# Kernel tuning notes

Measured on AMD Instinct MI355X. Metric: run time of the kernel, lower is better.

The kernel has to match this reference:

```python
import jax, jax.numpy as jnp
import numpy as np

B, N, D = 4, 4096, 3
Q = jnp.array([0.05, 0.95, 0.25, 0.75], dtype=jnp.float32)  # q_begin + q_end


def _nn_diff(S1, S2):
    # For each point in S1 find nearest point in S2 (squared L2), return S1 - closest_S2.
    # d2: [N, N] built via the ||a||^2 + ||b||^2 - 2ab expansion (avoids [N,N,D]).
    d2 = (jnp.sum(S1 * S1, axis=-1, keepdims=True)
          + jnp.sum(S2 * S2, axis=-1)[None, :]
          - 2.0 * (S1 @ S2.T))
    idx = jnp.argmin(d2, axis=1)          # [N] nearest index in S2
    return S1 - S2[idx]                   # [N, D] vector residuals (mean=False path)


def _masked_std(v, mask):
    # torch.std over the masked subset (unbiased, correction=1), mask is float {0,1}.
    n = jnp.sum(mask)
    mean = jnp.sum(v * mask) / n
    var = jnp.sum(mask * (v - mean) ** 2) / (n - 1.0)
    return jnp.sqrt(var)


def _mask_std_pair(d):
    # mask_by_Z: quantiles computed under no_grad (stop_gradient), then std of each subset.
    v = d.reshape(-1)
    q = jnp.quantile(jax.lax.stop_gradient(v), Q.astype(v.dtype))
    mask_begin = ((v < q[0]) | (v > q[1])).astype(v.dtype)
    mask_end = ((v > q[2]) & (v < q[3])).astype(v.dtype)
    return _masked_std(v, mask_begin), _masked_std(v, mask_end)


def _sigma_distance(S1, S2):
    d12 = _nn_diff(S1, S2)  # S1 -> S2 residuals
    d21 = _nn_diff(S2, S1)  # S2 -> S1 residuals
    b1, e1 = _mask_std_pair(d12)
    b2, e2 = _mask_std_pair(d21)
    return jnp.maximum(b1, b2), jnp.maximum(e1, e2)


def setup_inputs() -> dict:
    key = jax.random.key(0)
    kx, ky = jax.random.split(key)
    x = jax.random.normal(kx, (B, N, D), dtype=jnp.float32)
    y = jax.random.normal(ky, (B, N, D), dtype=jnp.float32)
    return {"x": x, "y": y}


def reference(x, y):
    begin, end = jax.vmap(_sigma_distance)(x, y)  # [B], [B]
    return begin.mean(), end.mean()
```

## Files before the change

kernel.cpp:

```cpp
#include <hip/hip_runtime.h>
#include <math.h>

constexpr int B_  = 4;
constexpr int N_  = 4096;
constexpr int NV  = N_ * 3;
constexpr int CCHUNK = 1024;
constexpr int NCH = N_ / CCHUNK;

__device__ inline unsigned f2k(float f) {
    unsigned b = __float_as_uint(f);
    return b ^ ((unsigned)((int)b >> 31) | 0x80000000u);
}
__device__ inline float k2f(unsigned k) {
    unsigned b = (k & 0x80000000u) ? (k ^ 0x80000000u) : ~k;
    return __uint_as_float(b);
}

__global__ __launch_bounds__(256) void nn_partial_kernel(const float* __restrict__ x,
                                                         const float* __restrict__ y,
                                                         float2* __restrict__ part) {
    __shared__ float4 s2[CCHUNK];
    const int pair = blockIdx.z;
    const int b    = pair >> 1;
    const int dir  = pair & 1;
    const float* S1 = (dir == 0 ? x : y) + b * NV;
    const float* S2 = (dir == 0 ? y : x) + b * NV;
    const int cbase = blockIdx.y * CCHUNK;

    for (int j = threadIdx.x; j < CCHUNK; j += 256) {
        float bx = S2[(cbase + j) * 3 + 0];
        float by = S2[(cbase + j) * 3 + 1];
        float bz = S2[(cbase + j) * 3 + 2];
        s2[j] = make_float4(bx, by, bz, bx * bx + by * by + bz * bz);
    }
    __syncthreads();

    const int q = blockIdx.x * 256 + threadIdx.x;
    const float ax = S1[q * 3 + 0];
    const float ay = S1[q * 3 + 1];
    const float az = S1[q * 3 + 2];

    float best = INFINITY;
    int bidx = 0;
    #pragma unroll 8
    for (int j = 0; j < CCHUNK; ++j) {
        float4 c = s2[j];
        float dot = ax * c.x + ay * c.y + az * c.z;
        float d2  = fmaf(-2.0f, dot, c.w);
        if (d2 < best) { best = d2; bidx = cbase + j; }
    }
    part[(pair * NCH + blockIdx.y) * N_ + q] = make_float2(best, (float)bidx);
}

__global__ __launch_bounds__(256) void nn_merge_kernel(const float* __restrict__ x,
                                                       const float* __restrict__ y,
                                                       const float2* __restrict__ part,
                                                       float* __restrict__ resid) {
    const int pair = blockIdx.y;
    const int b    = pair >> 1;
    const int dir  = pair & 1;
    const float* S1 = (dir == 0 ? x : y) + b * NV;
    const float* S2 = (dir == 0 ? y : x) + b * NV;
    const int q = blockIdx.x * 256 + threadIdx.x;

    float best = INFINITY;
    int bidx = 0;
    #pragma unroll
    for (int c = 0; c < NCH; ++c) {
        float2 p = part[(pair * NCH + c) * N_ + q];
        if (p.x < best) { best = p.x; bidx = (int)p.y; }
    }
    float* outp = resid + pair * NV + q * 3;
    outp[0] = S1[q * 3 + 0] - S2[bidx * 3 + 0];
    outp[1] = S1[q * 3 + 1] - S2[bidx * 3 + 1];
    outp[2] = S1[q * 3 + 2] - S2[bidx * 3 + 2];
}

__global__ __launch_bounds__(1024) void quantile_select_kernel(const float* __restrict__ resid,
                                                               float* __restrict__ qbuf) {
    __shared__ unsigned keys[NV];
    __shared__ int hist[256];
    __shared__ int s_sel, s_want, s_cnt;
    __shared__ unsigned s_min;

    const int t    = blockIdx.x & 3;
    const int pair = blockIdx.x >> 2;
    const int tid  = threadIdx.x;
    const float* v = resid + pair * NV;

    const float Qs[4] = {0.05f, 0.95f, 0.25f, 0.75f};
    const float pos = Qs[t] * (float)(NV - 1);
    const int   k0  = (int)floorf(pos);
    const float fr  = pos - (float)k0;

    for (int i = tid; i < NV; i += 1024) keys[i] = f2k(v[i]);
    __syncthreads();

    unsigned prefix = 0u, pmask = 0u;
    int want = k0;
    for (int shift = 24; shift >= 0; shift -= 8) {
        for (int i = tid; i < 256; i += 1024) hist[i] = 0;
        __syncthreads();
        for (int i = tid; i < NV; i += 1024) {
            unsigned k = keys[i];
            if ((k & pmask) == prefix) atomicAdd(&hist[(k >> shift) & 255], 1);
        }
        __syncthreads();
        if (tid < 64) {
            int c0 = hist[tid * 4 + 0], c1 = hist[tid * 4 + 1];
            int c2 = hist[tid * 4 + 2], c3 = hist[tid * 4 + 3];
            int s = c0 + c1 + c2 + c3;
            int pre = s;
            #pragma unroll
            for (int off = 1; off < 64; off <<= 1) {
                int u = __shfl_up(pre, off);
                if (tid >= off) pre += u;
            }
            int excl = pre - s;
            bool hit = (want >= excl) && (want < excl + s);
            unsigned long long m = __ballot(hit);
            int hl = (int)(__ffsll((unsigned long long)m) - 1);
            if (tid == hl) {
                int w = want - excl;
                int sel;
                if      (w < c0)           { sel = tid * 4 + 0; }
                else if (w < c0 + c1)      { sel = tid * 4 + 1; w -= c0; }
                else if (w < c0 + c1 + c2) { sel = tid * 4 + 2; w -= c0 + c1; }
                else                       { sel = tid * 4 + 3; w -= c0 + c1 + c2; }
                s_sel = sel; s_want = w;
            }
        }
        __syncthreads();
        prefix |= ((unsigned)s_sel) << shift;
        pmask  |= (0xFFu << shift);
        want = s_want;
        __syncthreads();
    }
    const unsigned key0 = prefix;
    const float v0 = k2f(key0);

    if (tid == 0) { s_cnt = 0; s_min = 0xFFFFFFFFu; }
    __syncthreads();
    int loc = 0; unsigned locmin = 0xFFFFFFFFu;
    for (int i = tid; i < NV; i += 1024) {
        unsigned k = keys[i];
        if (k <= key0) loc++;
        else if (k < locmin) locmin = k;
    }
    atomicAdd(&s_cnt, loc);
    atomicMin(&s_min, locmin);
    __syncthreads();
    if (tid == 0) {
        float v1 = (s_cnt >= k0 + 2) ? v0 : k2f(s_min);
        qbuf[pair * 4 + t] = v0 + fr * (v1 - v0);
    }
}

__global__ __launch_bounds__(1024) void masked_stats_kernel(const float* __restrict__ resid,
                                                            const float* __restrict__ qbuf,
                                                            float* __restrict__ stats) {
    __shared__ float red[64];
    __shared__ float sh[8];
    const int pair = blockIdx.x;
    const int tid  = threadIdx.x;
    const float* v = resid + pair * NV;
    const float q0 = qbuf[pair * 4 + 0], q1 = qbuf[pair * 4 + 1];
    const float q2 = qbuf[pair * 4 + 2], q3 = qbuf[pair * 4 + 3];

    float cb = 0.f, sb = 0.f, ce = 0.f, se = 0.f;
    for (int i = tid; i < NV; i += 1024) {
        float val = v[i];
        if ((val < q0) || (val > q1)) { cb += 1.f; sb += val; }
        if ((val > q2) && (val < q3)) { ce += 1.f; se += val; }
    }
    for (int off = 32; off > 0; off >>= 1) {
        cb += __shfl_down(cb, off);
        sb += __shfl_down(sb, off);
        ce += __shfl_down(ce, off);
        se += __shfl_down(se, off);
    }
    const int wid = tid >> 6, lane = tid & 63;
    if (lane == 0) {
        red[wid * 4 + 0] = cb; red[wid * 4 + 1] = sb;
        red[wid * 4 + 2] = ce; red[wid * 4 + 3] = se;
    }
    __syncthreads();
    if (tid == 0) {
        float tcb = 0.f, tsb = 0.f, tce = 0.f, tse = 0.f;
        for (int w = 0; w < 16; ++w) {
            tcb += red[w * 4 + 0]; tsb += red[w * 4 + 1];
            tce += red[w * 4 + 2]; tse += red[w * 4 + 3];
        }
        sh[0] = tsb / tcb;
        sh[1] = tse / tce;
        sh[2] = tcb;
        sh[3] = tce;
    }
    __syncthreads();
    const float mean_b = sh[0], mean_e = sh[1];
    const float nb = sh[2], ne = sh[3];

    float vb = 0.f, ve = 0.f;
    for (int i = tid; i < NV; i += 1024) {
        float val = v[i];
        if ((val < q0) || (val > q1)) { float d = val - mean_b; vb += d * d; }
        if ((val > q2) && (val < q3)) { float d = val - mean_e; ve += d * d; }
    }
    for (int off = 32; off > 0; off >>= 1) {
        vb += __shfl_down(vb, off);
        ve += __shfl_down(ve, off);
    }
    __syncthreads();
    if (lane == 0) { red[wid * 2 + 0] = vb; red[wid * 2 + 1] = ve; }
    __syncthreads();
    if (tid == 0) {
        float tvb = 0.f, tve = 0.f;
        for (int w = 0; w < 16; ++w) { tvb += red[w * 2 + 0]; tve += red[w * 2 + 1]; }
        stats[pair * 2 + 0] = sqrtf(tvb / (nb - 1.f));
        stats[pair * 2 + 1] = sqrtf(tve / (ne - 1.f));
    }
}

__global__ void final_kernel(const float* __restrict__ stats, float* __restrict__ out) {
    if (threadIdx.x == 0 && blockIdx.x == 0) {
        float sb = 0.f, se = 0.f;
        for (int b = 0; b < B_; ++b) {
            float b1 = stats[(b * 2 + 0) * 2 + 0];
            float b2 = stats[(b * 2 + 1) * 2 + 0];
            float e1 = stats[(b * 2 + 0) * 2 + 1];
            float e2 = stats[(b * 2 + 1) * 2 + 1];
            sb += fmaxf(b1, b2);
            se += fmaxf(e1, e2);
        }
        out[0] = sb / (float)B_;
        out[1] = se / (float)B_;
    }
}

extern "C" void kernel_launch(void* const* d_in, const int* in_sizes, int n_in,
                              void* d_out, int out_size, void* d_ws, size_t ws_size,
                              hipStream_t stream) {
    const float* x = (const float*)d_in[0];
    const float* y = (const float*)d_in[1];
    float* out = (float*)d_out;

    float*  resid = (float*)d_ws;
    float2* part  = (float2*)(resid + 8 * NV);
    float*  qbuf  = (float*)(part + 8 * NCH * N_);
    float*  stats = qbuf + 32;

    nn_partial_kernel<<<dim3(N_ / 256, NCH, 8), 256, 0, stream>>>(x, y, part);
    nn_merge_kernel<<<dim3(N_ / 256, 8), 256, 0, stream>>>(x, y, part, resid);
    quantile_select_kernel<<<32, 1024, 0, stream>>>(resid, qbuf);
    masked_stats_kernel<<<8, 1024, 0, stream>>>(resid, qbuf, stats);
    final_kernel<<<1, 64, 0, stream>>>(stats, out);
}
```

Baseline: 73.41 us.

## Register-tile NN search with 8 queries per thread and adaptive candidate split

The nearest-neighbour kernel now has each thread hold 8 query points in registers, loaded with float4 reads, and reuse every shared-memory candidate across all 8. Candidates are pre-scaled by -2 so the distance is a chain of three FMAs. The candidate dimension is split into up to 32 chunks, picked at launch from the workspace size, so the grid keeps enough blocks. The quantile and stats kernels drop to 256 threads, use vectorized float4 loads and reduce with wave shuffles instead of per-thread shared atomics. The costs are higher register pressure and a longer partial-result merge when there are more chunks.

```diff
diff --git a/kernel.cpp b/kernel.cpp
--- a/kernel.cpp
+++ b/kernel.cpp
@@ -4,8 +4,7 @@
 constexpr int B_  = 4;
 constexpr int N_  = 4096;
 constexpr int NV  = N_ * 3;
-constexpr int CCHUNK = 1024;
-constexpr int NCH = N_ / CCHUNK;
+constexpr int QPT = 8;
 
 __device__ inline unsigned f2k(float f) {
     unsigned b = __float_as_uint(f);
@@ -18,44 +17,69 @@
 
 __global__ __launch_bounds__(256) void nn_partial_kernel(const float* __restrict__ x,
                                                          const float* __restrict__ y,
-                                                         float2* __restrict__ part) {
-    __shared__ float4 s2[CCHUNK];
+                                                         float2* __restrict__ part,
+                                                         int ncch) {
+    __shared__ float4 s2[1024];
+    const int cch  = N_ / ncch;
     const int pair = blockIdx.z;
     const int b    = pair >> 1;
     const int dir  = pair & 1;
     const float* S1 = (dir == 0 ? x : y) + b * NV;
     const float* S2 = (dir == 0 ? y : x) + b * NV;
-    const int cbase = blockIdx.y * CCHUNK;
-
-    for (int j = threadIdx.x; j < CCHUNK; j += 256) {
+    const int cbase = blockIdx.x * cch;
+
+    for (int j = threadIdx.x; j < cch; j += 256) {
         float bx = S2[(cbase + j) * 3 + 0];
         float by = S2[(cbase + j) * 3 + 1];
         float bz = S2[(cbase + j) * 3 + 2];
-        s2[j] = make_float4(bx, by, bz, bx * bx + by * by + bz * bz);
-    }
-    __syncthreads();
-
-    const int q = blockIdx.x * 256 + threadIdx.x;
-    const float ax = S1[q * 3 + 0];
-    const float ay = S1[q * 3 + 1];
-    const float az = S1[q * 3 + 2];
-
-    float best = INFINITY;
-    int bidx = 0;
-    #pragma unroll 8
-    for (int j = 0; j < CCHUNK; ++j) {
+        s2[j] = make_float4(-2.f * bx, -2.f * by, -2.f * bz,
+                            bx * bx + by * by + bz * bz);
+    }
+    __syncthreads();
+
+    const int q0 = blockIdx.y * 2048 + threadIdx.x * QPT;
+    float ax[QPT], ay[QPT], az[QPT];
+    {
+        const float4* p4 = (const float4*)(S1 + q0 * 3);
+        float4 v[6];
+        #pragma unroll
+        for (int i = 0; i < 6; ++i) v[i] = p4[i];
+        const float* f = (const float*)v;
+        #pragma unroll
+        for (int k = 0; k < QPT; ++k) {
+            ax[k] = f[k * 3 + 0]; ay[k] = f[k * 3 + 1]; az[k] = f[k * 3 + 2];
+        }
+    }
+
+    float best[QPT]; int idx[QPT];
+    #pragma unroll
+    for (int k = 0; k < QPT; ++k) { best[k] = INFINITY; idx[k] = 0; }
+
+    #pragma unroll 2
+    for (int j = 0; j < cch; ++j) {
         float4 c = s2[j];
-        float dot = ax * c.x + ay * c.y + az * c.z;
-        float d2  = fmaf(-2.0f, dot, c.w);
-        if (d2 < best) { best = d2; bidx = cbase + j; }
-    }
-    part[(pair * NCH + blockIdx.y) * N_ + q] = make_float2(best, (float)bidx);
+        const int jg = cbase + j;
+        #pragma unroll
+        for (int k = 0; k < QPT; ++k) {
+            float d2 = fmaf(ax[k], c.x, fmaf(ay[k], c.y, fmaf(az[k], c.z, c.w)));
+            if (d2 < best[k]) idx[k] = jg;
+            best[k] = fminf(d2, best[k]);
+        }
+    }
+
+    float2 o[QPT];
+    #pragma unroll
+    for (int k = 0; k < QPT; ++k) o[k] = make_float2(best[k], (float)idx[k]);
+    float4* op = (float4*)(part + (size_t)(pair * ncch + blockIdx.x) * N_ + q0);
+    #pragma unroll
+    for (int i = 0; i < QPT / 2; ++i) op[i] = ((const float4*)o)[i];
 }
 
 __global__ __launch_bounds__(256) void nn_merge_kernel(const float* __restrict__ x,
                                                        const float* __restrict__ y,
                                                        const float2* __restrict__ part,
-                                                       float* __restrict__ resid) {
+                                                       float* __restrict__ resid,
+                                                       int ncch) {
     const int pair = blockIdx.y;
     const int b    = pair >> 1;
     const int dir  = pair & 1;
@@ -65,9 +89,8 @@
 
     float best = INFINITY;
     int bidx = 0;
-    #pragma unroll
-    for (int c = 0; c < NCH; ++c) {
-        float2 p = part[(pair * NCH + c) * N_ + q];
+    for (int c = 0; c < ncch; ++c) {
+        float2 p = part[(size_t)(pair * ncch + c) * N_ + q];
         if (p.x < best) { best = p.x; bidx = (int)p.y; }
     }
     float* outp = resid + pair * NV + q * 3;
@@ -76,8 +99,8 @@
     outp[2] = S1[q * 3 + 2] - S2[bidx * 3 + 2];
 }
 
-__global__ __launch_bounds__(1024) void quantile_select_kernel(const float* __restrict__ resid,
-                                                               float* __restrict__ qbuf) {
+__global__ __launch_bounds__(256) void quantile_select_kernel(const float* __restrict__ resid,
+                                                              float* __restrict__ qbuf) {
     __shared__ unsigned keys[NV];
     __shared__ int hist[256];
     __shared__ int s_sel, s_want, s_cnt;
@@ -86,22 +109,27 @@
     const int t    = blockIdx.x & 3;
     const int pair = blockIdx.x >> 2;
     const int tid  = threadIdx.x;
-    const float* v = resid + pair * NV;
+    const int lane = tid & 63;
 
     const float Qs[4] = {0.05f, 0.95f, 0.25f, 0.75f};
     const float pos = Qs[t] * (float)(NV - 1);
     const int   k0  = (int)floorf(pos);
     const float fr  = pos - (float)k0;
 
-    for (int i = tid; i < NV; i += 1024) keys[i] = f2k(v[i]);
+    const float4* v4 = (const float4*)(resid + pair * NV);
+    for (int i = tid; i < NV / 4; i += 256) {
+        float4 v = v4[i];
+        uint4 k = make_uint4(f2k(v.x), f2k(v.y), f2k(v.z), f2k(v.w));
+        ((uint4*)keys)[i] = k;
+    }
     __syncthreads();
 
     unsigned prefix = 0u, pmask = 0u;
     int want = k0;
     for (int shift = 24; shift >= 0; shift -= 8) {
-        for (int i = tid; i < 256; i += 1024) hist[i] = 0;
+        hist[tid] = 0;
         __syncthreads();
-        for (int i = tid; i < NV; i += 1024) {
+        for (int i = tid; i < NV; i += 256) {
             unsigned k = keys[i];
             if ((k & pmask) == prefix) atomicAdd(&hist[(k >> shift) & 255], 1);
         }
@@ -142,13 +170,17 @@
     if (tid == 0) { s_cnt = 0; s_min = 0xFFFFFFFFu; }
     __syncthreads();
     int loc = 0; unsigned locmin = 0xFFFFFFFFu;
-    for (int i = tid; i < NV; i += 1024) {
+    for (int i = tid; i < NV; i += 256) {
         unsigned k = keys[i];
         if (k <= key0) loc++;
         else if (k < locmin) locmin = k;
     }
-    atomicAdd(&s_cnt, loc);
-    atomicMin(&s_min, locmin);
+    for (int off = 32; off > 0; off >>= 1) {
+        loc += __shfl_down(loc, off);
+        unsigned m2 = __shfl_down(locmin, off);
+        locmin = (m2 < locmin) ? m2 : locmin;
+    }
+    if (lane == 0) { atomicAdd(&s_cnt, loc); atomicMin(&s_min, locmin); }
     __syncthreads();
     if (tid == 0) {
         float v1 = (s_cnt >= k0 + 2) ? v0 : k2f(s_min);
@@ -156,22 +188,28 @@
     }
 }
 
-__global__ __launch_bounds__(1024) void masked_stats_kernel(const float* __restrict__ resid,
-                                                            const float* __restrict__ qbuf,
-                                                            float* __restrict__ stats) {
-    __shared__ float red[64];
+__global__ __launch_bounds__(256) void masked_stats_kernel(const float* __restrict__ resid,
+                                                           const float* __restrict__ qbuf,
+                                                           float* __restrict__ stats) {
+    __shared__ float red[16];
     __shared__ float sh[8];
     const int pair = blockIdx.x;
     const int tid  = threadIdx.x;
-    const float* v = resid + pair * NV;
+    const int wid = tid >> 6, lane = tid & 63;
+    const float4* v4 = (const float4*)(resid + pair * NV);
     const float q0 = qbuf[pair * 4 + 0], q1 = qbuf[pair * 4 + 1];
     const float q2 = qbuf[pair * 4 + 2], q3 = qbuf[pair * 4 + 3];
 
     float cb = 0.f, sb = 0.f, ce = 0.f, se = 0.f;
-    for (int i = tid; i < NV; i += 1024) {
-        float val = v[i];
-        if ((val < q0) || (val > q1)) { cb += 1.f; sb += val; }
-        if ((val > q2) && (val < q3)) { ce += 1.f; se += val; }
+    for (int i = tid; i < NV / 4; i += 256) {
+        float4 v = v4[i];
+        float vals[4] = {v.x, v.y, v.z, v.w};
+        #pragma unroll
+        for (int u = 0; u < 4; ++u) {
+            float val = vals[u];
+            if ((val < q0) || (val > q1)) { cb += 1.f; sb += val; }
+            if ((val > q2) && (val < q3)) { ce += 1.f; se += val; }
+        }
     }
     for (int off = 32; off > 0; off >>= 1) {
         cb += __shfl_down(cb, off);
@@ -179,7 +217,6 @@
         ce += __shfl_down(ce, off);
         se += __shfl_down(se, off);
     }
-    const int wid = tid >> 6, lane = tid & 63;
     if (lane == 0) {
         red[wid * 4 + 0] = cb; red[wid * 4 + 1] = sb;
         red[wid * 4 + 2] = ce; red[wid * 4 + 3] = se;
@@ -187,7 +224,7 @@
     __syncthreads();
     if (tid == 0) {
         float tcb = 0.f, tsb = 0.f, tce = 0.f, tse = 0.f;
-        for (int w = 0; w < 16; ++w) {
+        for (int w = 0; w < 4; ++w) {
             tcb += red[w * 4 + 0]; tsb += red[w * 4 + 1];
             tce += red[w * 4 + 2]; tse += red[w * 4 + 3];
         }
@@ -201,10 +238,15 @@
     const float nb = sh[2], ne = sh[3];
 
     float vb = 0.f, ve = 0.f;
-    for (int i = tid; i < NV; i += 1024) {
-        float val = v[i];
-        if ((val < q0) || (val > q1)) { float d = val - mean_b; vb += d * d; }
-        if ((val > q2) && (val < q3)) { float d = val - mean_e; ve += d * d; }
+    for (int i = tid; i < NV / 4; i += 256) {
+        float4 v = v4[i];
+        float vals[4] = {v.x, v.y, v.z, v.w};
+        #pragma unroll
+        for (int u = 0; u < 4; ++u) {
+            float val = vals[u];
+            if ((val < q0) || (val > q1)) { float d = val - mean_b; vb += d * d; }
+            if ((val > q2) && (val < q3)) { float d = val - mean_e; ve += d * d; }
+        }
     }
     for (int off = 32; off > 0; off >>= 1) {
         vb += __shfl_down(vb, off);
@@ -215,7 +257,7 @@
     __syncthreads();
     if (tid == 0) {
         float tvb = 0.f, tve = 0.f;
-        for (int w = 0; w < 16; ++w) { tvb += red[w * 2 + 0]; tve += red[w * 2 + 1]; }
+        for (int w = 0; w < 4; ++w) { tvb += red[w * 2 + 0]; tve += red[w * 2 + 1]; }
         stats[pair * 2 + 0] = sqrtf(tvb / (nb - 1.f));
         stats[pair * 2 + 1] = sqrtf(tve / (ne - 1.f));
     }
@@ -245,13 +287,20 @@
     float* out = (float*)d_out;
 
     float*  resid = (float*)d_ws;
-    float2* part  = (float2*)(resid + 8 * NV);
-    float*  qbuf  = (float*)(part + 8 * NCH * N_);
+    float*  qbuf  = resid + 8 * NV;
     float*  stats = qbuf + 32;
-
-    nn_partial_kernel<<<dim3(N_ / 256, NCH, 8), 256, 0, stream>>>(x, y, part);
-    nn_merge_kernel<<<dim3(N_ / 256, 8), 256, 0, stream>>>(x, y, part, resid);
-    quantile_select_kernel<<<32, 1024, 0, stream>>>(resid, qbuf);
-    masked_stats_kernel<<<8, 1024, 0, stream>>>(resid, qbuf, stats);
+    float2* part  = (float2*)(stats + 16 + 16);
+
+    const size_t head = (size_t)(8 * NV + 64) * sizeof(float);
+    int ncch = 4;
+    for (int c = 32; c >= 4; c >>= 1) {
+        size_t need = head + (size_t)8 * c * N_ * sizeof(float2);
+        if (ws_size >= need) { ncch = c; break; }
+    }
+
+    nn_partial_kernel<<<dim3(ncch, 2, 8), 256, 0, stream>>>(x, y, part, ncch);
+    nn_merge_kernel<<<dim3(N_ / 256, 8), 256, 0, stream>>>(x, y, part, resid, ncch);
+    quantile_select_kernel<<<32, 256, 0, stream>>>(resid, qbuf);
+    masked_stats_kernel<<<8, 256, 0, stream>>>(resid, qbuf, stats);
     final_kernel<<<1, 64, 0, stream>>>(stats, out);
 }
```

Measured after the change: 80.33 us. 1.09x slower.
